# Kernel optimization log

Measured on AMD Instinct MI355X. Metric: run time of the kernel, lower is better.

The kernel has to match this reference:

```python
import jax, jax.numpy as jnp
import numpy as np

N_NODES = 50000
N_EDGES = 800000
D = 128  # node_dim == edge_dim == out_dim


def setup_inputs() -> dict:
    key = jax.random.key(0)
    ks = jax.random.split(key, 8)
    x = jax.random.normal(ks[0], (N_NODES, D), dtype=jnp.float32)
    edge_feat = jax.random.normal(ks[1], (N_EDGES, D), dtype=jnp.float32)
    src = jax.random.randint(ks[2], (N_EDGES,), 0, N_NODES)
    dst = jax.random.randint(ks[3], (N_EDGES,), 0, N_NODES)
    # xavier-ish init scales
    W_fc = jax.random.normal(ks[4], (D, D), dtype=jnp.float32) * (1.0 / np.sqrt(D))
    W_rel = jax.random.normal(ks[5], (D, 2 * D), dtype=jnp.float32) * (1.0 / np.sqrt(2 * D))
    b_rel = jnp.zeros((D,), dtype=jnp.float32)
    W_attn = jax.random.normal(ks[6], (1, 2 * D), dtype=jnp.float32) * (1.0 / np.sqrt(2 * D))
    return {"x": x, "edge_feat": edge_feat, "src": src, "dst": dst,
            "W_fc": W_fc, "W_rel": W_rel, "b_rel": b_rel, "W_attn": W_attn}


def reference(x, edge_feat, src, dst, W_fc, W_rel, b_rel, W_attn):
    n = x.shape[0]
    # z = fc(input), no bias
    z = x @ W_fc.T                                    # [N, D]
    z_src = z[src]                                    # [E, D] gather
    z_dst = z[dst]                                    # [E, D] gather
    # end = relation_fc(cat([edge_h, z_dst]))
    end = jnp.concatenate([edge_feat, z_dst], axis=1) @ W_rel.T + b_rel  # [E, D]
    # a = attn_fc(cat([z_src, end])); e = leaky_relu(a)
    a = (jnp.concatenate([z_src, end], axis=1) @ W_attn.T)[:, 0]         # [E]
    e = jax.nn.leaky_relu(a, negative_slope=0.01)
    # segment softmax over each destination node's mailbox
    m = jax.ops.segment_max(e, dst, num_segments=n)   # [N]
    ex = jnp.exp(e - m[dst])                          # [E]
    denom = jax.ops.segment_sum(ex, dst, num_segments=n)                 # [N]
    alpha = ex / denom[dst]                           # [E]
    # weighted scatter-sum of src z into dst
    h = jax.ops.segment_sum(alpha[:, None] * z_src, dst, num_segments=n)  # [N, D]
    return h
```

## Files before the change

### kernel.cpp

```cpp
#include <hip/hip_runtime.h>

#define D 128

__device__ __forceinline__ unsigned short f2bf(float f) {
    unsigned u = __float_as_uint(f);
    u += 0x7fffu + ((u >> 16) & 1u);
    return (unsigned short)(u >> 16);
}
__device__ __forceinline__ float bf_lo(unsigned u) { return __uint_as_float(u << 16); }
__device__ __forceinline__ float bf_hi(unsigned u) { return __uint_as_float(u & 0xffff0000u); }

__global__ __launch_bounds__(256) void g_and_count(
    const float* __restrict__ Wrel,
    const float* __restrict__ brel,
    const float* __restrict__ Wattn,
    const int* __restrict__ dst,
    float* __restrict__ gbuf,
    int* __restrict__ cnt, int E)
{
    if (blockIdx.x == 0) {
        int k = threadIdx.x;
        float acc = 0.f;
        for (int j = 0; j < 128; ++j)
            acc += Wattn[128 + j] * Wrel[j * 256 + k];
        gbuf[k] = acc;
        if (k == 0) {
            float c = 0.f;
            for (int j = 0; j < 128; ++j) c += Wattn[128 + j] * brel[j];
            gbuf[256] = c;
        }
    } else {
        int e = (blockIdx.x - 1) * 256 + threadIdx.x;
        if (e < E) atomicAdd(&cnt[dst[e]], 1);
    }
}

__global__ __launch_bounds__(256) void zgemm_pq(
    const float* __restrict__ x, const float* __restrict__ W,
    const float* __restrict__ attn, const float* __restrict__ gbuf,
    unsigned short* __restrict__ zb, float* __restrict__ pbuf,
    float* __restrict__ qbuf, int nrows)
{
    __shared__ float xs[64][132];
    __shared__ float ws[128][132];
    int tid = threadIdx.x;
    int row0 = blockIdx.x * 64;

    for (int i = tid; i < 128 * 32; i += 256) {
        int c = i >> 5, k4 = (i & 31) << 2;
        float4 v = *(const float4*)&W[c * 128 + k4];
        *(float4*)&ws[c][k4] = v;
    }
    for (int i = tid; i < 64 * 32; i += 256) {
        int r = i >> 5, k4 = (i & 31) << 2;
        int gr = row0 + r;
        float4 v = make_float4(0.f, 0.f, 0.f, 0.f);
        if (gr < nrows) v = *(const float4*)&x[(size_t)gr * D + k4];
        *(float4*)&xs[r][k4] = v;
    }
    __syncthreads();

    int tx = tid & 15, ty = tid >> 4;
    float acc[4][8] = {};
    for (int k = 0; k < 128; k += 4) {
        float4 xv[4], wv[8];
#pragma unroll
        for (int i = 0; i < 4; ++i) xv[i] = *(const float4*)&xs[ty * 4 + i][k];
#pragma unroll
        for (int j = 0; j < 8; ++j) wv[j] = *(const float4*)&ws[tx + 16 * j][k];
#pragma unroll
        for (int i = 0; i < 4; ++i)
#pragma unroll
            for (int j = 0; j < 8; ++j)
                acc[i][j] += xv[i].x * wv[j].x + xv[i].y * wv[j].y +
                             xv[i].z * wv[j].z + xv[i].w * wv[j].w;
    }

    float a1[8], g2[8];
#pragma unroll
    for (int j = 0; j < 8; ++j) {
        a1[j] = attn[tx + 16 * j];
        g2[j] = gbuf[128 + tx + 16 * j];
    }
#pragma unroll
    for (int i = 0; i < 4; ++i) {
        int gr = row0 + ty * 4 + i;
        if (gr >= nrows) continue;
        float ps = 0.f, qs = 0.f;
#pragma unroll
        for (int j = 0; j < 8; ++j) {
            zb[(size_t)gr * D + tx + 16 * j] = f2bf(acc[i][j]);
            ps += a1[j] * acc[i][j];
            qs += g2[j] * acc[i][j];
        }
#pragma unroll
        for (int off = 8; off >= 1; off >>= 1) {
            ps += __shfl_xor(ps, off);
            qs += __shfl_xor(qs, off);
        }
        if (tx == 0) { pbuf[gr] = ps; qbuf[gr] = qs; }
    }
}

__global__ __launch_bounds__(256) void partial_sums(
    const int* __restrict__ cnt, int* __restrict__ bsum, int N)
{
    __shared__ int ws_[4];
    int tid = threadIdx.x, lane = tid & 63, wid = tid >> 6;
    int i0 = blockIdx.x * 1024 + tid * 4;
    int s = 0;
#pragma unroll
    for (int j = 0; j < 4; ++j) s += (i0 + j < N) ? cnt[i0 + j] : 0;
#pragma unroll
    for (int off = 32; off >= 1; off >>= 1) s += __shfl_xor(s, off);
    if (lane == 0) ws_[wid] = s;
    __syncthreads();
    if (tid == 0) bsum[blockIdx.x] = ws_[0] + ws_[1] + ws_[2] + ws_[3];
}

__global__ __launch_bounds__(256) void scan_partials(
    const int* __restrict__ bsum, int* __restrict__ boffs, int nb)
{
    __shared__ int ws_[4];
    int tid = threadIdx.x, lane = tid & 63, wid = tid >> 6;
    int v = (tid < nb) ? bsum[tid] : 0;
    int incl = v;
#pragma unroll
    for (int off = 1; off < 64; off <<= 1) {
        int t = __shfl_up(incl, off);
        if (lane >= off) incl += t;
    }
    if (lane == 63) ws_[wid] = incl;
    __syncthreads();
    int woff = 0;
    for (int w = 0; w < wid; ++w) woff += ws_[w];
    if (tid < nb) boffs[tid] = woff + incl - v;
}

__global__ __launch_bounds__(256) void local_scan(
    const int* __restrict__ cnt, const int* __restrict__ boffs,
    int* __restrict__ offs, int* __restrict__ cursor, int N, int E)
{
    __shared__ int ws_[4];
    int tid = threadIdx.x, lane = tid & 63, wid = tid >> 6;
    int i0 = blockIdx.x * 1024 + tid * 4;
    int v[4];
    int tsum = 0;
#pragma unroll
    for (int j = 0; j < 4; ++j) {
        v[j] = (i0 + j < N) ? cnt[i0 + j] : 0;
        tsum += v[j];
    }
    int incl = tsum;
#pragma unroll
    for (int off = 1; off < 64; off <<= 1) {
        int t = __shfl_up(incl, off);
        if (lane >= off) incl += t;
    }
    if (lane == 63) ws_[wid] = incl;
    __syncthreads();
    int woff = 0;
    for (int w = 0; w < wid; ++w) woff += ws_[w];
    int run = boffs[blockIdx.x] + woff + incl - tsum;
#pragma unroll
    for (int j = 0; j < 4; ++j) {
        if (i0 + j < N) { offs[i0 + j] = run; cursor[i0 + j] = run; }
        run += v[j];
    }
    if (blockIdx.x == 0 && tid == 0) offs[N] = E;
}

__global__ __launch_bounds__(256) void edge_logits_scatter(
    const float* __restrict__ ef,
    const int* __restrict__ src, const int* __restrict__ dst,
    const float* __restrict__ gbuf,
    const float* __restrict__ pbuf, const float* __restrict__ qbuf,
    int* __restrict__ cursor, int2* __restrict__ spack, int E)
{
    int tid = threadIdx.x;
    int lane = tid & 15;
    int e = blockIdx.x * 16 + (tid >> 4);
    if (e >= E) return;
    const float* efr = ef + (size_t)e * D;
    float acc = 0.f;
#pragma unroll
    for (int p = 0; p < 2; ++p) {
        int idx = lane * 4 + p * 64;
        float4 a4  = *(const float4*)&efr[idx];
        float4 g14 = *(const float4*)&gbuf[idx];
        acc += a4.x * g14.x + a4.y * g14.y + a4.z * g14.z + a4.w * g14.w;
    }
#pragma unroll
    for (int off = 8; off >= 1; off >>= 1) acc += __shfl_xor(acc, off);
    if (lane == 0) {
        int s = src[e], d = dst[e];
        float a = acc + pbuf[s] + qbuf[d] + gbuf[256];
        float ev = a > 0.f ? a : 0.01f * a;
        int pos = atomicAdd(&cursor[d], 1);
        spack[pos] = make_int2(s, __float_as_int(__expf(ev)));
    }
}

__global__ __launch_bounds__(256) void node_gather(
    const unsigned short* __restrict__ zb, const int2* __restrict__ spack,
    const int* __restrict__ offs, float* __restrict__ out, int N)
{
    int tid = threadIdx.x, half = tid & 31;
    int node = blockIdx.x * 8 + (tid >> 5);
    if (node >= N) return;
    int o0 = offs[node], o1 = offs[node + 1];
    float4 acc = make_float4(0.f, 0.f, 0.f, 0.f);
    float denom = 0.f;
    int j = o0;
    for (; j + 1 < o1; j += 2) {
        int2 p0 = spack[j], p1 = spack[j + 1];
        uint2 u0 = *(const uint2*)&zb[(size_t)p0.x * D + half * 4];
        uint2 u1 = *(const uint2*)&zb[(size_t)p1.x * D + half * 4];
        float x0 = __int_as_float(p0.y), x1 = __int_as_float(p1.y);
        denom += x0 + x1;
        acc.x += x0 * bf_lo(u0.x) + x1 * bf_lo(u1.x);
        acc.y += x0 * bf_hi(u0.x) + x1 * bf_hi(u1.x);
        acc.z += x0 * bf_lo(u0.y) + x1 * bf_lo(u1.y);
        acc.w += x0 * bf_hi(u0.y) + x1 * bf_hi(u1.y);
    }
    if (j < o1) {
        int2 p0 = spack[j];
        uint2 u0 = *(const uint2*)&zb[(size_t)p0.x * D + half * 4];
        float x0 = __int_as_float(p0.y);
        denom += x0;
        acc.x += x0 * bf_lo(u0.x);
        acc.y += x0 * bf_hi(u0.x);
        acc.z += x0 * bf_lo(u0.y);
        acc.w += x0 * bf_hi(u0.y);
    }
    if (o1 > o0) {
        float inv = 1.f / denom;
        acc.x *= inv; acc.y *= inv; acc.z *= inv; acc.w *= inv;
    }
    *(float4*)&out[(size_t)node * D + half * 4] = acc;
}

extern "C" void kernel_launch(void* const* d_in, const int* in_sizes, int n_in,
                              void* d_out, int out_size, void* d_ws, size_t ws_size,
                              hipStream_t stream) {
    const float* x     = (const float*)d_in[0];
    const float* ef    = (const float*)d_in[1];
    const int*   src   = (const int*)d_in[2];
    const int*   dst   = (const int*)d_in[3];
    const float* Wfc   = (const float*)d_in[4];
    const float* Wrel  = (const float*)d_in[5];
    const float* brel  = (const float*)d_in[6];
    const float* Wattn = (const float*)d_in[7];
    int N = in_sizes[0] / D;
    int E = in_sizes[2];
    int nb = (N + 1023) / 1024;
    float* out = (float*)d_out;

    unsigned short* zb = (unsigned short*)d_ws;
    int2*  spack  = (int2*)(zb + (size_t)N * D);
    float* pbuf   = (float*)(spack + E);
    float* qbuf   = pbuf + N;
    int*   cnt    = (int*)(qbuf + N);
    int*   cursor = cnt + N;
    int*   offs   = cursor + N;
    int*   bsum   = offs + N + 16;
    int*   boffs  = bsum + 256;
    float* gbuf   = (float*)(boffs + 256);

    hipMemsetAsync(cnt, 0, (size_t)N * sizeof(int), stream);

    g_and_count<<<1 + (E + 255) / 256, 256, 0, stream>>>(Wrel, brel, Wattn, dst,
                                                         gbuf, cnt, E);
    zgemm_pq<<<(N + 63) / 64, 256, 0, stream>>>(x, Wfc, Wattn, gbuf, zb, pbuf,
                                                qbuf, N);
    partial_sums<<<nb, 256, 0, stream>>>(cnt, bsum, N);
    scan_partials<<<1, 256, 0, stream>>>(bsum, boffs, nb);
    local_scan<<<nb, 256, 0, stream>>>(cnt, boffs, offs, cursor, N, E);
    edge_logits_scatter<<<(E + 15) / 16, 256, 0, stream>>>(ef, src, dst, gbuf,
                                                           pbuf, qbuf, cursor,
                                                           spack, E);
    node_gather<<<(N + 7) / 8, 256, 0, stream>>>(zb, spack, offs, out, N);
}
```

Baseline: 257.4 us.

## Fuse count into GEMM, merge scan kernels, widen gather loads

Replaces the memset with zeroing in an init kernel and moves the dst degree counting into extra blocks of the z GEMM launch. The three scan kernels become a single one in which each block recomputes its prefix by summing all earlier counts. The node gather now has 16 lanes per node, each loading 16 bytes (8 bf16), with 16 nodes per block. Together these cut the number of launches and make gather loads wider, at the cost of redundant prefix reads (quadratic in block count, small for about 49 blocks) and a mixed-role GEMM launch.

```diff
diff --git a/kernel.cpp b/kernel.cpp
--- a/kernel.cpp
+++ b/kernel.cpp
@@ -10,13 +10,12 @@
 __device__ __forceinline__ float bf_lo(unsigned u) { return __uint_as_float(u << 16); }
 __device__ __forceinline__ float bf_hi(unsigned u) { return __uint_as_float(u & 0xffff0000u); }
 
-__global__ __launch_bounds__(256) void g_and_count(
+__global__ __launch_bounds__(256) void g_init(
     const float* __restrict__ Wrel,
     const float* __restrict__ brel,
     const float* __restrict__ Wattn,
-    const int* __restrict__ dst,
     float* __restrict__ gbuf,
-    int* __restrict__ cnt, int E)
+    int* __restrict__ cnt, int N)
 {
     if (blockIdx.x == 0) {
         int k = threadIdx.x;
@@ -30,20 +29,27 @@
             gbuf[256] = c;
         }
     } else {
-        int e = (blockIdx.x - 1) * 256 + threadIdx.x;
-        if (e < E) atomicAdd(&cnt[dst[e]], 1);
-    }
-}
-
-__global__ __launch_bounds__(256) void zgemm_pq(
+        int i = (blockIdx.x - 1) * 256 + threadIdx.x;
+        if (i < N) cnt[i] = 0;
+    }
+}
+
+__global__ __launch_bounds__(256) void zgemm_pq_count(
     const float* __restrict__ x, const float* __restrict__ W,
     const float* __restrict__ attn, const float* __restrict__ gbuf,
     unsigned short* __restrict__ zb, float* __restrict__ pbuf,
-    float* __restrict__ qbuf, int nrows)
+    float* __restrict__ qbuf, int nrows,
+    const int* __restrict__ dst, int* __restrict__ cnt, int E, int nzb)
 {
     __shared__ float xs[64][132];
     __shared__ float ws[128][132];
     int tid = threadIdx.x;
+
+    if (blockIdx.x >= nzb) {
+        int e = (blockIdx.x - nzb) * 256 + tid;
+        if (e < E) atomicAdd(&cnt[dst[e]], 1);
+        return;
+    }
     int row0 = blockIdx.x * 64;
 
     for (int i = tid; i < 128 * 32; i += 256) {
@@ -102,29 +108,32 @@
     }
 }
 
-__global__ __launch_bounds__(256) void partial_sums(
-    const int* __restrict__ cnt, int* __restrict__ bsum, int N)
+__global__ __launch_bounds__(256) void fused_scan(
+    const int* __restrict__ cnt, int* __restrict__ offs,
+    int* __restrict__ cursor, int N, int E)
 {
     __shared__ int ws_[4];
     int tid = threadIdx.x, lane = tid & 63, wid = tid >> 6;
-    int i0 = blockIdx.x * 1024 + tid * 4;
+
+    int limit = blockIdx.x * 1024;
     int s = 0;
-#pragma unroll
-    for (int j = 0; j < 4; ++j) s += (i0 + j < N) ? cnt[i0 + j] : 0;
+    for (int i = tid; i < limit; i += 256) s += cnt[i];
 #pragma unroll
     for (int off = 32; off >= 1; off >>= 1) s += __shfl_xor(s, off);
     if (lane == 0) ws_[wid] = s;
     __syncthreads();
-    if (tid == 0) bsum[blockIdx.x] = ws_[0] + ws_[1] + ws_[2] + ws_[3];
-}
-
-__global__ __launch_bounds__(256) void scan_partials(
-    const int* __restrict__ bsum, int* __restrict__ boffs, int nb)
-{
-    __shared__ int ws_[4];
-    int tid = threadIdx.x, lane = tid & 63, wid = tid >> 6;
-    int v = (tid < nb) ? bsum[tid] : 0;
-    int incl = v;
+    int prefix = ws_[0] + ws_[1] + ws_[2] + ws_[3];
+    __syncthreads();
+
+    int i0 = blockIdx.x * 1024 + tid * 4;
+    int v[4];
+    int tsum = 0;
+#pragma unroll
+    for (int j = 0; j < 4; ++j) {
+        v[j] = (i0 + j < N) ? cnt[i0 + j] : 0;
+        tsum += v[j];
+    }
+    int incl = tsum;
 #pragma unroll
     for (int off = 1; off < 64; off <<= 1) {
         int t = __shfl_up(incl, off);
@@ -134,34 +143,7 @@
     __syncthreads();
     int woff = 0;
     for (int w = 0; w < wid; ++w) woff += ws_[w];
-    if (tid < nb) boffs[tid] = woff + incl - v;
-}
-
-__global__ __launch_bounds__(256) void local_scan(
-    const int* __restrict__ cnt, const int* __restrict__ boffs,
-    int* __restrict__ offs, int* __restrict__ cursor, int N, int E)
-{
-    __shared__ int ws_[4];
-    int tid = threadIdx.x, lane = tid & 63, wid = tid >> 6;
-    int i0 = blockIdx.x * 1024 + tid * 4;
-    int v[4];
-    int tsum = 0;
-#pragma unroll
-    for (int j = 0; j < 4; ++j) {
-        v[j] = (i0 + j < N) ? cnt[i0 + j] : 0;
-        tsum += v[j];
-    }
-    int incl = tsum;
-#pragma unroll
-    for (int off = 1; off < 64; off <<= 1) {
-        int t = __shfl_up(incl, off);
-        if (lane >= off) incl += t;
-    }
-    if (lane == 63) ws_[wid] = incl;
-    __syncthreads();
-    int woff = 0;
-    for (int w = 0; w < wid; ++w) woff += ws_[w];
-    int run = boffs[blockIdx.x] + woff + incl - tsum;
+    int run = prefix + woff + incl - tsum;
 #pragma unroll
     for (int j = 0; j < 4; ++j) {
         if (i0 + j < N) { offs[i0 + j] = run; cursor[i0 + j] = run; }
@@ -205,39 +187,47 @@
     const unsigned short* __restrict__ zb, const int2* __restrict__ spack,
     const int* __restrict__ offs, float* __restrict__ out, int N)
 {
-    int tid = threadIdx.x, half = tid & 31;
-    int node = blockIdx.x * 8 + (tid >> 5);
+    int tid = threadIdx.x, l = tid & 15;
+    int node = blockIdx.x * 16 + (tid >> 4);
     if (node >= N) return;
     int o0 = offs[node], o1 = offs[node + 1];
-    float4 acc = make_float4(0.f, 0.f, 0.f, 0.f);
+    float acc[8] = {};
     float denom = 0.f;
     int j = o0;
     for (; j + 1 < o1; j += 2) {
         int2 p0 = spack[j], p1 = spack[j + 1];
-        uint2 u0 = *(const uint2*)&zb[(size_t)p0.x * D + half * 4];
-        uint2 u1 = *(const uint2*)&zb[(size_t)p1.x * D + half * 4];
+        uint4 u0 = *(const uint4*)&zb[(size_t)p0.x * D + l * 8];
+        uint4 u1 = *(const uint4*)&zb[(size_t)p1.x * D + l * 8];
         float x0 = __int_as_float(p0.y), x1 = __int_as_float(p1.y);
         denom += x0 + x1;
-        acc.x += x0 * bf_lo(u0.x) + x1 * bf_lo(u1.x);
-        acc.y += x0 * bf_hi(u0.x) + x1 * bf_hi(u1.x);
-        acc.z += x0 * bf_lo(u0.y) + x1 * bf_lo(u1.y);
-        acc.w += x0 * bf_hi(u0.y) + x1 * bf_hi(u1.y);
+        acc[0] += x0 * bf_lo(u0.x) + x1 * bf_lo(u1.x);
+        acc[1] += x0 * bf_hi(u0.x) + x1 * bf_hi(u1.x);
+        acc[2] += x0 * bf_lo(u0.y) + x1 * bf_lo(u1.y);
+        acc[3] += x0 * bf_hi(u0.y) + x1 * bf_hi(u1.y);
+        acc[4] += x0 * bf_lo(u0.z) + x1 * bf_lo(u1.z);
+        acc[5] += x0 * bf_hi(u0.z) + x1 * bf_hi(u1.z);
+        acc[6] += x0 * bf_lo(u0.w) + x1 * bf_lo(u1.w);
+        acc[7] += x0 * bf_hi(u0.w) + x1 * bf_hi(u1.w);
     }
     if (j < o1) {
         int2 p0 = spack[j];
-        uint2 u0 = *(const uint2*)&zb[(size_t)p0.x * D + half * 4];
+        uint4 u0 = *(const uint4*)&zb[(size_t)p0.x * D + l * 8];
         float x0 = __int_as_float(p0.y);
         denom += x0;
-        acc.x += x0 * bf_lo(u0.x);
-        acc.y += x0 * bf_hi(u0.x);
-        acc.z += x0 * bf_lo(u0.y);
-        acc.w += x0 * bf_hi(u0.y);
-    }
-    if (o1 > o0) {
-        float inv = 1.f / denom;
-        acc.x *= inv; acc.y *= inv; acc.z *= inv; acc.w *= inv;
-    }
-    *(float4*)&out[(size_t)node * D + half * 4] = acc;
+        acc[0] += x0 * bf_lo(u0.x);
+        acc[1] += x0 * bf_hi(u0.x);
+        acc[2] += x0 * bf_lo(u0.y);
+        acc[3] += x0 * bf_hi(u0.y);
+        acc[4] += x0 * bf_lo(u0.z);
+        acc[5] += x0 * bf_hi(u0.z);
+        acc[6] += x0 * bf_lo(u0.w);
+        acc[7] += x0 * bf_hi(u0.w);
+    }
+    float inv = (o1 > o0) ? 1.f / denom : 0.f;
+    float4 v0 = make_float4(acc[0] * inv, acc[1] * inv, acc[2] * inv, acc[3] * inv);
+    float4 v1 = make_float4(acc[4] * inv, acc[5] * inv, acc[6] * inv, acc[7] * inv);
+    *(float4*)&out[(size_t)node * D + l * 8]     = v0;
+    *(float4*)&out[(size_t)node * D + l * 8 + 4] = v1;
 }
 
 extern "C" void kernel_launch(void* const* d_in, const int* in_sizes, int n_in,
@@ -253,7 +243,8 @@
     const float* Wattn = (const float*)d_in[7];
     int N = in_sizes[0] / D;
     int E = in_sizes[2];
-    int nb = (N + 1023) / 1024;
+    int nb  = (N + 1023) / 1024;
+    int nzb = (N + 63) / 64;
     float* out = (float*)d_out;
 
     unsigned short* zb = (unsigned short*)d_ws;
@@ -263,21 +254,15 @@
     int*   cnt    = (int*)(qbuf + N);
     int*   cursor = cnt + N;
     int*   offs   = cursor + N;
-    int*   bsum   = offs + N + 16;
-    int*   boffs  = bsum + 256;
-    float* gbuf   = (float*)(boffs + 256);
-
-    hipMemsetAsync(cnt, 0, (size_t)N * sizeof(int), stream);
-
-    g_and_count<<<1 + (E + 255) / 256, 256, 0, stream>>>(Wrel, brel, Wattn, dst,
-                                                         gbuf, cnt, E);
-    zgemm_pq<<<(N + 63) / 64, 256, 0, stream>>>(x, Wfc, Wattn, gbuf, zb, pbuf,
-                                                qbuf, N);
-    partial_sums<<<nb, 256, 0, stream>>>(cnt, bsum, N);
-    scan_partials<<<1, 256, 0, stream>>>(bsum, boffs, nb);
-    local_scan<<<nb, 256, 0, stream>>>(cnt, boffs, offs, cursor, N, E);
+    float* gbuf   = (float*)(offs + N + 16);
+
+    g_init<<<1 + (N + 255) / 256, 256, 0, stream>>>(Wrel, brel, Wattn, gbuf,
+                                                    cnt, N);
+    zgemm_pq_count<<<nzb + (E + 255) / 256, 256, 0, stream>>>(
+        x, Wfc, Wattn, gbuf, zb, pbuf, qbuf, N, dst, cnt, E, nzb);
+    fused_scan<<<nb, 256, 0, stream>>>(cnt, offs, cursor, N, E);
     edge_logits_scatter<<<(E + 15) / 16, 256, 0, stream>>>(ef, src, dst, gbuf,
                                                            pbuf, qbuf, cursor,
                                                            spack, E);
-    node_gather<<<(N + 7) / 8, 256, 0, stream>>>(zb, spack, offs, out, N);
-}
+    node_gather<<<(N + 15) / 16, 256, 0, stream>>>(zb, spack, offs, out, N);
+}
```

New measurement: 262.0 us. About the same (+1.8%).
